# Kernel tuning notes

Measured on AMD Instinct MI355X. Metric: run time of the kernel, lower is better.

Reference implementation:

```python
import jax, jax.numpy as jnp
import numpy as np


def setup_inputs() -> dict:
    key = jax.random.key(0)
    k1, k2, k3 = jax.random.split(key, 3)
    B, T1, T2, D = 16, 1024, 1024, 256
    x = jax.random.normal(k1, (B, T1, D), dtype=jnp.float32)
    y = jax.random.normal(k2, (B, T2, D), dtype=jnp.float32)
    WS = jax.random.normal(k3, (3 * D,), dtype=jnp.float32) * 0.05
    return {"x": x, "y": y, "WS": WS}


def reference(x, y, WS):
    # BiDAF trilinear similarity. Original computes
    #   S[b,i,j] = sum_k concat([x_i, 1, x_i])_k * concat([1, y_j, y_j])_k * WS_k
    # which decomposes exactly into:
    #   S = x @ w1 (broadcast over j) + y @ w2 (broadcast over i) + (x * w3) @ y^T
    D = x.shape[-1]
    w1, w2, w3 = WS[:D], WS[D:2 * D], WS[2 * D:]
    term_x = jnp.einsum('bid,d->bi', x, w1)            # [B, T1]
    term_y = jnp.einsum('bjd,d->bj', y, w2)            # [B, T2]
    term_xy = jnp.einsum('bid,bjd->bij', x * w3, y)    # [B, T1, T2]
    return term_xy + term_x[:, :, None] + term_y[:, None, :]
```

## Files before the change

kernel.cpp:

```cpp
#include <hip/hip_runtime.h>

#define DK 256
#define TT 1024
#define NB 16

typedef __attribute__((ext_vector_type(8))) short bf16x8;
typedef __attribute__((ext_vector_type(8))) unsigned short u16x8;
typedef __attribute__((ext_vector_type(4))) float f32x4;

__device__ __forceinline__ unsigned short f2bf(float f) {
    unsigned int u = __float_as_uint(f);
    unsigned int r = 0x7fffu + ((u >> 16) & 1u);
    return (unsigned short)((u + r) >> 16);
}

__global__ __launch_bounds__(256, 2) void fused_kernel(
    const float* __restrict__ x, const float* __restrict__ y,
    const float* __restrict__ WS, float* __restrict__ out)
{
    __shared__ unsigned short Bs[128 * DK];
    __shared__ float tys[128];

    const int tid  = threadIdx.x;
    const int lane = tid & 63;
    const int w    = tid >> 6;
    const int jt = blockIdx.x;
    const int is = blockIdx.y;
    const int b  = blockIdx.z;

    {
        const int j = tid >> 1;
        const int h = tid & 1;
        const float* gY  = y + ((size_t)b * TT + jt * 128 + j) * DK + h * 128;
        const float* w3p = WS + 2 * DK + h * 128;
        const float* w2p = WS + DK + h * 128;
        unsigned short* Brow = Bs + j * DK;
        float typ = 0.f;
        #pragma unroll
        for (int c = 0; c < 16; ++c) {
            const int d0 = c * 8;
            const float4 ya = *(const float4*)(gY + d0);
            const float4 yb = *(const float4*)(gY + d0 + 4);
            const float4 wa = *(const float4*)(w3p + d0);
            const float4 wb = *(const float4*)(w3p + d0 + 4);
            const float4 va = *(const float4*)(w2p + d0);
            const float4 vb = *(const float4*)(w2p + d0 + 4);
            typ += ya.x * va.x + ya.y * va.y + ya.z * va.z + ya.w * va.w
                 + yb.x * vb.x + yb.y * vb.y + yb.z * vb.z + yb.w * vb.w;
            u16x8 o;
            o[0] = f2bf(ya.x * wa.x); o[1] = f2bf(ya.y * wa.y);
            o[2] = f2bf(ya.z * wa.z); o[3] = f2bf(ya.w * wa.w);
            o[4] = f2bf(yb.x * wb.x); o[5] = f2bf(yb.y * wb.y);
            o[6] = f2bf(yb.z * wb.z); o[7] = f2bf(yb.w * wb.w);
            const int cg   = h * 16 + c;
            const int slot = cg ^ (j & 7);
            *(u16x8*)(Brow + slot * 8) = o;
        }
        typ += __shfl_xor(typ, 1);
        if (h == 0) tys[j] = typ;
    }
    __syncthreads();

    const int mfr  = lane & 15;
    const int quad = lane >> 4;
    const int i0   = is * 256 + w * 64;
    const float* gA = x + ((size_t)b * TT + i0) * DK;

    f32x4 acc[4][8];
    #pragma unroll
    for (int it = 0; it < 4; ++it)
        #pragma unroll
        for (int n = 0; n < 8; ++n)
            acc[it][n] = (f32x4){0.f, 0.f, 0.f, 0.f};
    float txp[4] = {0.f, 0.f, 0.f, 0.f};

    #pragma unroll
    for (int ks = 0; ks < 8; ++ks) {
        const float* w1p = WS + ks * 32 + quad * 8;
        const float4 w1a = *(const float4*)(w1p);
        const float4 w1b = *(const float4*)(w1p + 4);
        bf16x8 av[4];
        #pragma unroll
        for (int it = 0; it < 4; ++it) {
            const float* rp = gA + (size_t)(it * 16 + mfr) * DK
                              + ks * 32 + quad * 8;
            const float4 xa = *(const float4*)rp;
            const float4 xb = *(const float4*)(rp + 4);
            txp[it] += xa.x * w1a.x + xa.y * w1a.y + xa.z * w1a.z + xa.w * w1a.w
                     + xb.x * w1b.x + xb.y * w1b.y + xb.z * w1b.z + xb.w * w1b.w;
            bf16x8 a;
            a[0] = (short)f2bf(xa.x); a[1] = (short)f2bf(xa.y);
            a[2] = (short)f2bf(xa.z); a[3] = (short)f2bf(xa.w);
            a[4] = (short)f2bf(xb.x); a[5] = (short)f2bf(xb.y);
            a[6] = (short)f2bf(xb.z); a[7] = (short)f2bf(xb.w);
            av[it] = a;
        }
        #pragma unroll
        for (int n = 0; n < 8; ++n) {
            const int j    = n * 16 + mfr;
            const int slot = (ks * 4 + quad) ^ (j & 7);
            const bf16x8 bv = *(const bf16x8*)(Bs + j * DK + slot * 8);
            #pragma unroll
            for (int it = 0; it < 4; ++it)
                acc[it][n] = __builtin_amdgcn_mfma_f32_16x16x32_bf16(
                    av[it], bv, acc[it][n], 0, 0, 0);
        }
    }

    #pragma unroll
    for (int it = 0; it < 4; ++it) {
        txp[it] += __shfl_xor(txp[it], 16);
        txp[it] += __shfl_xor(txp[it], 32);
    }

    float tyv[8];
    #pragma unroll
    for (int n = 0; n < 8; ++n)
        tyv[n] = tys[n * 16 + mfr];

    float* outB = out + ((size_t)b << 20) + (size_t)i0 * TT + jt * 128;
    #pragma unroll
    for (int it = 0; it < 4; ++it) {
        #pragma unroll
        for (int r = 0; r < 4; ++r) {
            const int row = it * 16 + quad * 4 + r;
            const float trow = __shfl(txp[it], (lane & 48) | (quad * 4 + r));
            #pragma unroll
            for (int n = 0; n < 8; ++n)
                outB[(size_t)row * TT + n * 16 + mfr] =
                    acc[it][n][r] + trow + tyv[n];
        }
    }
}

extern "C" void kernel_launch(void* const* d_in, const int* in_sizes, int n_in,
                              void* d_out, int out_size, void* d_ws, size_t ws_size,
                              hipStream_t stream)
{
    const float* x  = (const float*)d_in[0];
    const float* y  = (const float*)d_in[1];
    const float* WS = (const float*)d_in[2];
    float* out = (float*)d_out;
    (void)d_ws; (void)ws_size;

    fused_kernel<<<dim3(8, 4, NB), dim3(256), 0, stream>>>(x, y, WS, out);
}
```

Baseline: 122.3 us.

## Use 512-thread blocks with smaller per-wave tiles and coalesced Y staging

Doubles the block to 8 waves, each computing a 32x128 output slice instead of 64x128, which halves the accumulator registers and raises the occupancy target to 4 blocks per CU. The Y staging loop is rewritten so 32 consecutive threads cover one row with contiguous 8-float chunks, giving coalesced loads; the row dot product for w2 is reduced with a shuffle tree. The grid is flattened to 1D with the batch index in the low bits, changing the block scheduling order. In exchange, each B tile in shared memory is now reused by more waves, but each A element does less MFMA work per load.

```diff
diff --git a/kernel.cpp b/kernel.cpp
--- a/kernel.cpp
+++ b/kernel.cpp
@@ -14,7 +14,7 @@
     return (unsigned short)((u + r) >> 16);
 }
 
-__global__ __launch_bounds__(256, 2) void fused_kernel(
+__global__ __launch_bounds__(512, 4) void fused_kernel(
     const float* __restrict__ x, const float* __restrict__ y,
     const float* __restrict__ WS, float* __restrict__ out)
 {
@@ -24,64 +24,68 @@
     const int tid  = threadIdx.x;
     const int lane = tid & 63;
     const int w    = tid >> 6;
-    const int jt = blockIdx.x;
-    const int is = blockIdx.y;
-    const int b  = blockIdx.z;
+
+    const int id = blockIdx.x;
+    const int b  = id & 15;
+    const int is = (id >> 4) & 3;
+    const int jt = id >> 6;
 
     {
-        const int j = tid >> 1;
-        const int h = tid & 1;
-        const float* gY  = y + ((size_t)b * TT + jt * 128 + j) * DK + h * 128;
-        const float* w3p = WS + 2 * DK + h * 128;
-        const float* w2p = WS + DK + h * 128;
-        unsigned short* Brow = Bs + j * DK;
-        float typ = 0.f;
+        const float* gY0 = y + ((size_t)b * TT + jt * 128) * DK;
         #pragma unroll
-        for (int c = 0; c < 16; ++c) {
-            const int d0 = c * 8;
-            const float4 ya = *(const float4*)(gY + d0);
-            const float4 yb = *(const float4*)(gY + d0 + 4);
-            const float4 wa = *(const float4*)(w3p + d0);
-            const float4 wb = *(const float4*)(w3p + d0 + 4);
-            const float4 va = *(const float4*)(w2p + d0);
-            const float4 vb = *(const float4*)(w2p + d0 + 4);
-            typ += ya.x * va.x + ya.y * va.y + ya.z * va.z + ya.w * va.w
-                 + yb.x * vb.x + yb.y * vb.y + yb.z * vb.z + yb.w * vb.w;
+        for (int it = 0; it < 8; ++it) {
+            const int g = it * 512 + tid;
+            const int j = g >> 5;
+            const int c = g & 31;
+            const float* gY  = gY0 + (size_t)j * DK + c * 8;
+            const float* w3p = WS + 2 * DK + c * 8;
+            const float* w2p = WS + DK + c * 8;
+            const float4 ya = *(const float4*)(gY);
+            const float4 yb = *(const float4*)(gY + 4);
+            const float4 wa = *(const float4*)(w3p);
+            const float4 wb = *(const float4*)(w3p + 4);
+            const float4 va = *(const float4*)(w2p);
+            const float4 vb = *(const float4*)(w2p + 4);
+            float p = ya.x * va.x + ya.y * va.y + ya.z * va.z + ya.w * va.w
+                    + yb.x * vb.x + yb.y * vb.y + yb.z * vb.z + yb.w * vb.w;
             u16x8 o;
             o[0] = f2bf(ya.x * wa.x); o[1] = f2bf(ya.y * wa.y);
             o[2] = f2bf(ya.z * wa.z); o[3] = f2bf(ya.w * wa.w);
             o[4] = f2bf(yb.x * wb.x); o[5] = f2bf(yb.y * wb.y);
             o[6] = f2bf(yb.z * wb.z); o[7] = f2bf(yb.w * wb.w);
-            const int cg   = h * 16 + c;
-            const int slot = cg ^ (j & 7);
-            *(u16x8*)(Brow + slot * 8) = o;
+            const int slot = c ^ (j & 7);
+            *(u16x8*)(Bs + j * DK + slot * 8) = o;
+            p += __shfl_xor(p, 1);
+            p += __shfl_xor(p, 2);
+            p += __shfl_xor(p, 4);
+            p += __shfl_xor(p, 8);
+            p += __shfl_xor(p, 16);
+            if ((tid & 31) == 0) tys[j] = p;
         }
-        typ += __shfl_xor(typ, 1);
-        if (h == 0) tys[j] = typ;
     }
     __syncthreads();
 
     const int mfr  = lane & 15;
     const int quad = lane >> 4;
-    const int i0   = is * 256 + w * 64;
+    const int i0   = is * 256 + w * 32;
     const float* gA = x + ((size_t)b * TT + i0) * DK;
 
-    f32x4 acc[4][8];
+    f32x4 acc[2][8];
     #pragma unroll
-    for (int it = 0; it < 4; ++it)
+    for (int it = 0; it < 2; ++it)
         #pragma unroll
         for (int n = 0; n < 8; ++n)
             acc[it][n] = (f32x4){0.f, 0.f, 0.f, 0.f};
-    float txp[4] = {0.f, 0.f, 0.f, 0.f};
+    float txp[2] = {0.f, 0.f};
 
     #pragma unroll
     for (int ks = 0; ks < 8; ++ks) {
         const float* w1p = WS + ks * 32 + quad * 8;
         const float4 w1a = *(const float4*)(w1p);
         const float4 w1b = *(const float4*)(w1p + 4);
-        bf16x8 av[4];
+        bf16x8 av[2];
         #pragma unroll
-        for (int it = 0; it < 4; ++it) {
+        for (int it = 0; it < 2; ++it) {
             const float* rp = gA + (size_t)(it * 16 + mfr) * DK
                               + ks * 32 + quad * 8;
             const float4 xa = *(const float4*)rp;
@@ -101,14 +105,14 @@
             const int slot = (ks * 4 + quad) ^ (j & 7);
             const bf16x8 bv = *(const bf16x8*)(Bs + j * DK + slot * 8);
             #pragma unroll
-            for (int it = 0; it < 4; ++it)
+            for (int it = 0; it < 2; ++it)
                 acc[it][n] = __builtin_amdgcn_mfma_f32_16x16x32_bf16(
                     av[it], bv, acc[it][n], 0, 0, 0);
         }
     }
 
     #pragma unroll
-    for (int it = 0; it < 4; ++it) {
+    for (int it = 0; it < 2; ++it) {
         txp[it] += __shfl_xor(txp[it], 16);
         txp[it] += __shfl_xor(txp[it], 32);
     }
@@ -120,7 +124,7 @@
 
     float* outB = out + ((size_t)b << 20) + (size_t)i0 * TT + jt * 128;
     #pragma unroll
-    for (int it = 0; it < 4; ++it) {
+    for (int it = 0; it < 2; ++it) {
         #pragma unroll
         for (int r = 0; r < 4; ++r) {
             const int row = it * 16 + quad * 4 + r;
@@ -143,5 +147,5 @@
     float* out = (float*)d_out;
     (void)d_ws; (void)ws_size;
 
-    fused_kernel<<<dim3(8, 4, NB), dim3(256), 0, stream>>>(x, y, WS, out);
+    fused_kernel<<<dim3(512), dim3(512), 0, stream>>>(x, y, WS, out);
 }
```

New measurement: 109.6 us. 10.3% less time.
